# Performance work log

Hardware: AMD Instinct MI355X
Metric: run time of the kernel (lower is better)

Reference implementation:

```python
import jax, jax.numpy as jnp
import numpy as np

D_MODEL = 512
NUM_HEADS = 8
QUERY_GROUPS = 2
HEAD_DIM = D_MODEL // NUM_HEADS  # 64
ROPE_THETA = 10000.0
SCALE = 0.125  # 1/sqrt(head_dim)
NEG_INF = -1e9


def setup_inputs() -> dict:
    key = jax.random.key(0)
    k1, k2, k3 = jax.random.split(key, 3)
    B, T, S = 2, 512, 16
    x = jax.random.normal(k1, (B, T, S, D_MODEL), jnp.float32)
    padding_mask = jnp.ones((B, T * S), jnp.int32)  # [B, T*H*W], all valid
    qkv_dim = NUM_HEADS * HEAD_DIM + 2 * QUERY_GROUPS * HEAD_DIM  # 768
    qkv_w = jax.random.normal(k2, (qkv_dim, D_MODEL), jnp.float32) / np.float32(np.sqrt(D_MODEL))
    o_w = jax.random.normal(k3, (D_MODEL, NUM_HEADS * HEAD_DIM), jnp.float32) / np.float32(np.sqrt(D_MODEL))
    return {"x": x, "padding_mask": padding_mask, "qkv_w": qkv_w, "o_w": o_w}


def _rope(v, pos):
    # v: [N, T, h, d]; classic RoPE (rotate-half) over temporal positions
    half = v.shape[-1] // 2
    inv_freq = 1.0 / (ROPE_THETA ** (jnp.arange(0, half, dtype=jnp.float32) / half))
    ang = pos[:, None] * inv_freq  # [T, half]
    cos = jnp.cos(ang)[None, :, None, :]
    sin = jnp.sin(ang)[None, :, None, :]
    v1, v2 = v[..., :half], v[..., half:]
    return jnp.concatenate([v1 * cos - v2 * sin, v1 * sin + v2 * cos], axis=-1)


def reference(x, padding_mask, qkv_w, o_w):
    B, T, S, D = x.shape
    # temporal attention: flatten spatial patches into batch -> [B*S, T, D]
    xt = x.transpose(0, 2, 1, 3).reshape(B * S, T, D)
    qkv = xt @ qkv_w.T  # [B*S, T, (H+2G)*hd]
    q_end = NUM_HEADS * HEAD_DIM
    k_end = q_end + QUERY_GROUPS * HEAD_DIM
    q = qkv[..., :q_end].reshape(B * S, T, NUM_HEADS, HEAD_DIM)
    k = qkv[..., q_end:k_end].reshape(B * S, T, QUERY_GROUPS, HEAD_DIM)
    v = qkv[..., k_end:].reshape(B * S, T, QUERY_GROUPS, HEAD_DIM)
    pos = jnp.arange(T, dtype=jnp.float32)
    q = _rope(q, pos)
    k = _rope(k, pos)
    # GQA: broadcast each KV group to its query heads
    rep = NUM_HEADS // QUERY_GROUPS
    k = jnp.repeat(k, rep, axis=2)
    v = jnp.repeat(v, rep, axis=2)
    scores = jnp.einsum('nqhd,nkhd->nhqk', q, k) * SCALE  # [B*S, H, T, T]
    causal = jnp.tril(jnp.ones((T, T), bool))
    pm = padding_mask.astype(bool).reshape(-1, T)  # [B*S, T] query-side mask (as in torch path)
    mask = causal[None, None, :, :] & pm[:, None, :, None]
    scores = jnp.where(mask, scores, NEG_INF)
    attn = jax.nn.softmax(scores, axis=-1)
    out = jnp.einsum('nhqk,nkhd->nqhd', attn, v).reshape(B * S, T, D)
    out = out @ o_w.T  # output projection
    return out.reshape(B, S, T, D).transpose(0, 2, 1, 3)  # back to [B, T, S, D]
```

## Files before the change

kernel.cpp:

```cpp
#include <hip/hip_runtime.h>
#include <hip/hip_bf16.h>

typedef __attribute__((ext_vector_type(8))) short bf16x8;
typedef __attribute__((ext_vector_type(4))) float f32x4;
typedef __attribute__((ext_vector_type(4))) short s16x4;

#define DM 512
#define T_SEQ 512
#define NSEQ 32
#define MROWS 16384
#define QKV_DIM 768
#define HD 64
#define NEG_INF_F (-1000000000.0f)
#define LOG2E 1.44269504088896340736f

__device__ __forceinline__ short f2bf(float f) {
    unsigned int u = __builtin_bit_cast(unsigned int, f);
    unsigned int r = (u + 0x7FFFu + ((u >> 16) & 1u)) >> 16;
    return (short)r;
}

__device__ __forceinline__ short f2bf_hw(float f) {
    __hip_bfloat16 h = __float2bfloat16(f);
    return __builtin_bit_cast(short, h);
}

__device__ __forceinline__ void gload16(const void* g, void* l) {
    __builtin_amdgcn_global_load_lds(
        (const __attribute__((address_space(1))) void*)g,
        (__attribute__((address_space(3))) void*)l, 16, 0, 0);
}

__global__ __launch_bounds__(128) void k_convert(
    const float* __restrict__ x, const float* __restrict__ qkvw, const float* __restrict__ owf,
    short* __restrict__ xt, short* __restrict__ qw, short* __restrict__ ow,
    float* __restrict__ cosT, float* __restrict__ sinT)
{
    int bidx = blockIdx.x, tid = threadIdx.x;
    if (bidx < MROWS) {
        int m = bidx; int n = m >> 9, t = m & 511, b = n >> 4, s = n & 15;
        const float* src = x + ((size_t)((b * 512 + t) * 16 + s)) * 512;
        float4 v = *(const float4*)(src + tid * 4);
        s16x4 o; o.x = f2bf(v.x); o.y = f2bf(v.y); o.z = f2bf(v.z); o.w = f2bf(v.w);
        *(s16x4*)(xt + (size_t)m * 512 + tid * 4) = o;
    } else if (bidx < MROWS + 1280) {
        int wr = bidx - MROWS;
        const float* src; short* dst;
        if (wr < QKV_DIM) { src = qkvw + (size_t)wr * 512; dst = qw + (size_t)wr * 512; }
        else             { src = owf + (size_t)(wr - QKV_DIM) * 512; dst = ow + (size_t)(wr - QKV_DIM) * 512; }
        float4 v = *(const float4*)(src + tid * 4);
        s16x4 o; o.x = f2bf(v.x); o.y = f2bf(v.y); o.z = f2bf(v.z); o.w = f2bf(v.w);
        *(s16x4*)(dst + tid * 4) = o;
    } else {
        int idx = (bidx - (MROWS + 1280)) * 128 + tid;
        int t = idx >> 5, d = idx & 31;
        float inv = powf(10000.0f, -(float)d * (1.0f / 32.0f));
        float ang = (float)t * inv;
        float sv, cv; sincosf(ang, &sv, &cv);
        cosT[idx] = cv; sinT[idx] = sv;
    }
}

__device__ __forceinline__ void gemm_mainloop(
    const short* __restrict__ Ab, const short* __restrict__ Bb, int K,
    short* As, short* Bs, int wave, int lane, f32x4 acc[4][4])
{
    int wr = (wave >> 1) * 64, wc = (wave & 1) * 64;
    for (int kt = 0; kt < K; kt += 32) {
        __syncthreads();
        #pragma unroll
        for (int c = 0; c < 2; ++c) {
            int chunk = (wave * 2 + c) * 64 + lane;
            int row = chunk >> 2, kc = chunk & 3;
            gload16(Ab + (size_t)row * K + kt + kc * 8, As + (wave * 2 + c) * 512);
            gload16(Bb + (size_t)row * K + kt + kc * 8, Bs + (wave * 2 + c) * 512);
        }
        __syncthreads();
        bf16x8 af[4], bg[4];
        #pragma unroll
        for (int mf = 0; mf < 4; ++mf)
            af[mf] = *(const bf16x8*)(As + (wr + mf * 16 + (lane & 15)) * 32 + ((lane >> 4) << 3));
        #pragma unroll
        for (int nf = 0; nf < 4; ++nf)
            bg[nf] = *(const bf16x8*)(Bs + (wc + nf * 16 + (lane & 15)) * 32 + ((lane >> 4) << 3));
        #pragma unroll
        for (int mf = 0; mf < 4; ++mf)
            #pragma unroll
            for (int nf = 0; nf < 4; ++nf)
                acc[mf][nf] = __builtin_amdgcn_mfma_f32_16x16x32_bf16(af[mf], bg[nf], acc[mf][nf], 0, 0, 0);
    }
}

__global__ __launch_bounds__(256) void k_gemm_qkv(
    const short* __restrict__ xt, const short* __restrict__ qw,
    const float* __restrict__ cosT, const float* __restrict__ sinT,
    short* __restrict__ qb, short* __restrict__ kb, short* __restrict__ vtb)
{
    __shared__ short As[128 * 32], Bs[128 * 32];
    int tid = threadIdx.x, wave = tid >> 6, lane = tid & 63;
    int bm = blockIdx.x, bn = blockIdx.y;
    f32x4 acc[4][4] = {};
    gemm_mainloop(xt + (size_t)bm * 128 * 512, qw + (size_t)bn * 128 * 512, 512, As, Bs, wave, lane, acc);

    const float QSC = 0.125f * LOG2E;
    int wr = (wave >> 1) * 64, wc = (wave & 1) * 64;
    int gbase = bn * 128 + wc;
    int cl = lane & 15;
    #pragma unroll
    for (int mf = 0; mf < 4; ++mf) {
        #pragma unroll
        for (int rg = 0; rg < 4; ++rg) {
            int r = bm * 128 + wr + mf * 16 + ((lane >> 4) << 2) + rg;
            int n = r >> 9, t = r & 511;
            #pragma unroll
            for (int nf = 0; nf < 2; ++nf) {
                int dlo = nf * 16 + cl;
                float v1 = acc[mf][nf][rg];
                float v2 = acc[mf][nf + 2][rg];
                if (gbase < 512) {
                    int h = gbase >> 6;
                    float c = cosT[t * 32 + dlo], s = sinT[t * 32 + dlo];
                    size_t base = ((size_t)(n * 8 + h) * 512 + t) * 64;
                    qb[base + dlo]      = f2bf((v1 * c - v2 * s) * QSC);
                    qb[base + dlo + 32] = f2bf((v1 * s + v2 * c) * QSC);
                } else if (gbase < 640) {
                    int g = (gbase - 512) >> 6;
                    float c = cosT[t * 32 + dlo], s = sinT[t * 32 + dlo];
                    size_t base = ((size_t)(n * 2 + g) * 512 + t) * 64;
                    kb[base + dlo]      = f2bf(v1 * c - v2 * s);
                    kb[base + dlo + 32] = f2bf(v1 * s + v2 * c);
                } else {
                    int g = (gbase - 640) >> 6;
                    size_t base = ((size_t)(n * 2 + g) * 64) * 512;
                    vtb[base + (size_t)dlo * 512 + t]        = f2bf(v1);
                    vtb[base + (size_t)(dlo + 32) * 512 + t] = f2bf(v2);
                }
            }
        }
    }
}

__global__ __launch_bounds__(256) void k_attn(
    const short* __restrict__ qb, const short* __restrict__ kb, const short* __restrict__ vtb,
    const int* __restrict__ pm, short* __restrict__ ao)
{
    __shared__ short Kt[2][64 * 64];
    __shared__ short Vt[2][64 * 64];
    __shared__ short Pws[4][16 * 64];
    int tid = threadIdx.x, wave = tid >> 6, lane = tid & 63;
    int cl = lane & 15, g = lane >> 4;
    int bid = blockIdx.x;
    int c = bid & 3, h = (bid >> 2) & 7, n = bid >> 5;
    int kg = h >> 2;
    const short* Qb = qb + ((size_t)(n * 8 + h) * 512) * 64;
    const short* Kb = kb + ((size_t)(n * 2 + kg) * 512) * 64;
    const short* Vb = vtb + ((size_t)(n * 2 + kg) * 64) * 512;

    int rowb0 = c * 64 + wave * 16;
    int rowb1 = (7 - c) * 64 + wave * 16;

    bf16x8 qf[2][2];
    #pragma unroll
    for (int mf = 0; mf < 2; ++mf)
        #pragma unroll
        for (int ks = 0; ks < 2; ++ks)
            qf[mf][ks] = *(const bf16x8*)(Qb + (size_t)((mf ? rowb1 : rowb0) + cl) * 64 + ks * 32 + (g << 3));

    f32x4 Oc[2][4] = {};
    float mrow[2] = { -1e30f, -1e30f };
    float lrow[2] = { 0.f, 0.f };
    bool rvalid[2];
    rvalid[0] = pm[n * 512 + rowb0 + cl] != 0;
    rvalid[1] = pm[n * 512 + rowb1 + cl] != 0;

    auto stage = [&](int jt, int buf) {
        int c0 = jt * 64;
        #pragma unroll
        for (int cc = 0; cc < 2; ++cc) {
            int chunk = (wave * 2 + cc) * 64 + lane;
            int row = chunk >> 3, kc = chunk & 7;
            int sw = (kc ^ (row & 7)) << 3;
            gload16(Kb + (size_t)(c0 + row) * 64 + sw, &Kt[buf][(wave * 2 + cc) * 512]);
            gload16(Vb + (size_t)row * 512 + c0 + sw, &Vt[buf][(wave * 2 + cc) * 512]);
        }
    };

    int NT = 8 - c;
    stage(0, 0);
    for (int jt = 0; jt < NT; ++jt) {
        __syncthreads();
        if (jt + 1 < NT) stage(jt + 1, (jt + 1) & 1);
        int c0 = jt * 64;
        bool act0 = (jt <= c);
        const short* Kc = Kt[jt & 1];
        const short* Vc = Vt[jt & 1];

        f32x4 sacc[2][4] = {};
        #pragma unroll
        for (int ks = 0; ks < 2; ++ks) {
            bf16x8 kf[4];
            #pragma unroll
            for (int nf = 0; nf < 4; ++nf) {
                int row = nf * 16 + cl;
                int kc = ks * 4 + g;
                kf[nf] = *(const bf16x8*)(Kc + row * 64 + ((kc ^ (row & 7)) << 3));
            }
            #pragma unroll
            for (int mf = 0; mf < 2; ++mf) {
                if (mf == 0 && !act0) continue;
                #pragma unroll
                for (int nf = 0; nf < 4; ++nf)
                    sacc[mf][nf] = __builtin_amdgcn_mfma_f32_16x16x32_bf16(kf[nf], qf[mf][ks], sacc[mf][nf], 0, 0, 0);
            }
        }

        #pragma unroll
        for (int mf = 0; mf < 2; ++mf) {
            if (mf == 0 && !act0) continue;
            const bool diag = mf ? (jt == NT - 1) : (jt == c);
            int rq = (mf ? rowb1 : rowb0) + cl;
            float rmax = -1e30f;
            if (diag) {
                #pragma unroll
                for (int nf = 0; nf < 4; ++nf)
                    #pragma unroll
                    for (int rg = 0; rg < 4; ++rg) {
                        int kv = c0 + nf * 16 + g * 4 + rg;
                        float sv = sacc[mf][nf][rg];
                        sv = (kv <= rq && rvalid[mf]) ? sv : NEG_INF_F;
                        sacc[mf][nf][rg] = sv;
                        rmax = fmaxf(rmax, sv);
                    }
            } else {
                #pragma unroll
                for (int nf = 0; nf < 4; ++nf)
                    #pragma unroll
                    for (int rg = 0; rg < 4; ++rg)
                        rmax = fmaxf(rmax, sacc[mf][nf][rg]);
            }
            rmax = fmaxf(rmax, __shfl_xor(rmax, 16));
            rmax = fmaxf(rmax, __shfl_xor(rmax, 32));
            float mold = mrow[mf];
            int defer = __all(rmax - mold <= 8.0f);
            float mnew = defer ? mold : fmaxf(mold, rmax);
            mrow[mf] = mnew;
            float rsum = 0.f;
            #pragma unroll
            for (int nf = 0; nf < 4; ++nf) {
                s16x4 pk;
                #pragma unroll
                for (int rg = 0; rg < 4; ++rg) {
                    float p = exp2f(sacc[mf][nf][rg] - mnew);
                    rsum += p;
                    ((short*)&pk)[rg] = f2bf_hw(p);
                }
                *(s16x4*)(&Pws[wave][cl * 64 + ((((nf << 1) + (g >> 1)) ^ (cl & 7)) << 3) + ((g & 1) << 2)]) = pk;
            }
            rsum += __shfl_xor(rsum, 16);
            rsum += __shfl_xor(rsum, 32);
            if (defer) {
                lrow[mf] += rsum;
            } else {
                float alpha = exp2f(mold - mnew);
                lrow[mf] = lrow[mf] * alpha + rsum;
                #pragma unroll
                for (int rg = 0; rg < 4; ++rg) {
                    float av = __shfl(alpha, (lane & 48) + (g << 2) + rg);
                    #pragma unroll
                    for (int nf = 0; nf < 4; ++nf) Oc[mf][nf][rg] *= av;
                }
            }
            #pragma unroll
            for (int ks = 0; ks < 2; ++ks) {
                bf16x8 vf[4];
                #pragma unroll
                for (int nf = 0; nf < 4; ++nf) {
                    int row = nf * 16 + cl;
                    int kc = ks * 4 + g;
                    vf[nf] = *(const bf16x8*)(Vc + row * 64 + ((kc ^ (row & 7)) << 3));
                }
                bf16x8 pf = *(const bf16x8*)(&Pws[wave][cl * 64 + (((ks * 4 + g) ^ (cl & 7)) << 3)]);
                #pragma unroll
                for (int nf = 0; nf < 4; ++nf)
                    Oc[mf][nf] = __builtin_amdgcn_mfma_f32_16x16x32_bf16(pf, vf[nf], Oc[mf][nf], 0, 0, 0);
            }
        }
    }

    #pragma unroll
    for (int mf = 0; mf < 2; ++mf)
        #pragma unroll
        for (int rg = 0; rg < 4; ++rg) {
            float li = __shfl(lrow[mf], (lane & 48) + (g << 2) + rg);
            float inv = 1.0f / li;
            int r = (mf ? rowb1 : rowb0) + g * 4 + rg;
            size_t base = ((size_t)n * 512 + r) * 512 + h * 64;
            #pragma unroll
            for (int nf = 0; nf < 4; ++nf)
                ao[base + nf * 16 + cl] = f2bf_hw(Oc[mf][nf][rg] * inv);
        }
}

__global__ __launch_bounds__(256) void k_gemm_out(
    const short* __restrict__ ao, const short* __restrict__ ow, float* __restrict__ out)
{
    __shared__ short As[128 * 32], Bs[128 * 32];
    int tid = threadIdx.x, wave = tid >> 6, lane = tid & 63;
    int bm = blockIdx.x, bn = blockIdx.y;
    f32x4 acc[4][4] = {};
    gemm_mainloop(ao + (size_t)bm * 128 * 512, ow + (size_t)bn * 128 * 512, 512, As, Bs, wave, lane, acc);

    int wr = (wave >> 1) * 64, wc = (wave & 1) * 64;
    #pragma unroll
    for (int mf = 0; mf < 4; ++mf) {
        #pragma unroll
        for (int rg = 0; rg < 4; ++rg) {
            int r = bm * 128 + wr + mf * 16 + ((lane >> 4) << 2) + rg;
            int n = r >> 9, t = r & 511, b = n >> 4, s = n & 15;
            size_t obase = ((size_t)((b * 512 + t) * 16 + s)) * 512;
            #pragma unroll
            for (int nf = 0; nf < 4; ++nf) {
                int ccc = bn * 128 + wc + nf * 16 + (lane & 15);
                out[obase + ccc] = acc[mf][nf][rg];
            }
        }
    }
}

extern "C" void kernel_launch(void* const* d_in, const int* in_sizes, int n_in,
                              void* d_out, int out_size, void* d_ws, size_t ws_size,
                              hipStream_t stream) {
    (void)in_sizes; (void)n_in; (void)out_size; (void)ws_size;
    const float* x    = (const float*)d_in[0];
    const int*   pmsk = (const int*)d_in[1];
    const float* qkvw = (const float*)d_in[2];
    const float* owf  = (const float*)d_in[3];
    char* ws = (char*)d_ws;
    short* xt   = (short*)(ws + 0);
    short* qw   = (short*)(ws + 16777216);
    short* ow   = (short*)(ws + 17563648);
    float* cosT = (float*)(ws + 18087936);
    float* sinT = (float*)(ws + 18153472);
    short* qbuf = (short*)(ws + 18219008);
    short* kbuf = (short*)(ws + 34996224);
    short* vtbuf= (short*)(ws + 39190528);
    short* aobuf = xt;
    float* out = (float*)d_out;

    k_convert<<<dim3(17792), dim3(128), 0, stream>>>(x, qkvw, owf, xt, qw, ow, cosT, sinT);
    k_gemm_qkv<<<dim3(128, 6), dim3(256), 0, stream>>>(xt, qw, cosT, sinT, qbuf, kbuf, vtbuf);
    k_attn<<<dim3(1024), dim3(256), 0, stream>>>(qbuf, kbuf, vtbuf, pmsk, aobuf);
    k_gemm_out<<<dim3(128, 4), dim3(256), 0, stream>>>(aobuf, ow, out);
}
```

Before: 94.73 us.

## Process paired query tiles in two sequential phases to cut register pressure

```diff
diff --git a/kernel.cpp b/kernel.cpp
--- a/kernel.cpp
+++ b/kernel.cpp
@@ -156,23 +156,6 @@
     const short* Kb = kb + ((size_t)(n * 2 + kg) * 512) * 64;
     const short* Vb = vtb + ((size_t)(n * 2 + kg) * 64) * 512;
 
-    int rowb0 = c * 64 + wave * 16;
-    int rowb1 = (7 - c) * 64 + wave * 16;
-
-    bf16x8 qf[2][2];
-    #pragma unroll
-    for (int mf = 0; mf < 2; ++mf)
-        #pragma unroll
-        for (int ks = 0; ks < 2; ++ks)
-            qf[mf][ks] = *(const bf16x8*)(Qb + (size_t)((mf ? rowb1 : rowb0) + cl) * 64 + ks * 32 + (g << 3));
-
-    f32x4 Oc[2][4] = {};
-    float mrow[2] = { -1e30f, -1e30f };
-    float lrow[2] = { 0.f, 0.f };
-    bool rvalid[2];
-    rvalid[0] = pm[n * 512 + rowb0 + cl] != 0;
-    rvalid[1] = pm[n * 512 + rowb1 + cl] != 0;
-
     auto stage = [&](int jt, int buf) {
         int c0 = jt * 64;
         #pragma unroll
@@ -185,40 +168,43 @@
         }
     };
 
-    int NT = 8 - c;
     stage(0, 0);
-    for (int jt = 0; jt < NT; ++jt) {
-        __syncthreads();
-        if (jt + 1 < NT) stage(jt + 1, (jt + 1) & 1);
-        int c0 = jt * 64;
-        bool act0 = (jt <= c);
-        const short* Kc = Kt[jt & 1];
-        const short* Vc = Vt[jt & 1];
-
-        f32x4 sacc[2][4] = {};
-        #pragma unroll
-        for (int ks = 0; ks < 2; ++ks) {
-            bf16x8 kf[4];
-            #pragma unroll
-            for (int nf = 0; nf < 4; ++nf) {
-                int row = nf * 16 + cl;
-                int kc = ks * 4 + g;
-                kf[nf] = *(const bf16x8*)(Kc + row * 64 + ((kc ^ (row & 7)) << 3));
-            }
-            #pragma unroll
-            for (int mf = 0; mf < 2; ++mf) {
-                if (mf == 0 && !act0) continue;
-                #pragma unroll
-                for (int nf = 0; nf < 4; ++nf)
-                    sacc[mf][nf] = __builtin_amdgcn_mfma_f32_16x16x32_bf16(kf[nf], qf[mf][ks], sacc[mf][nf], 0, 0, 0);
-            }
-        }
-
-        #pragma unroll
-        for (int mf = 0; mf < 2; ++mf) {
-            if (mf == 0 && !act0) continue;
-            const bool diag = mf ? (jt == NT - 1) : (jt == c);
-            int rq = (mf ? rowb1 : rowb0) + cl;
+    int buf = 0;
+    #pragma unroll
+    for (int ph = 0; ph < 2; ++ph) {
+        int rowb = (ph ? (7 - c) : c) * 64 + wave * 16;
+        int NTp = ph ? (8 - c) : (c + 1);
+        bf16x8 qf[2];
+        #pragma unroll
+        for (int ks = 0; ks < 2; ++ks)
+            qf[ks] = *(const bf16x8*)(Qb + (size_t)(rowb + cl) * 64 + ks * 32 + (g << 3));
+        f32x4 Oc[4] = {};
+        float mrow = -1e30f, lrow = 0.f;
+        bool rv = pm[n * 512 + rowb + cl] != 0;
+        int rq = rowb + cl;
+
+        for (int jt = 0; jt < NTp; ++jt) {
+            __syncthreads();
+            if (jt + 1 < NTp) stage(jt + 1, buf ^ 1);
+            else if (ph == 0) stage(0, buf ^ 1);
+            int c0 = jt * 64;
+            const short* Kc = Kt[buf];
+            const short* Vc = Vt[buf];
+            buf ^= 1;
+
+            f32x4 sacc[4] = {};
+            #pragma unroll
+            for (int ks = 0; ks < 2; ++ks) {
+                #pragma unroll
+                for (int nf = 0; nf < 4; ++nf) {
+                    int row = nf * 16 + cl;
+                    int kc = ks * 4 + g;
+                    bf16x8 kf = *(const bf16x8*)(Kc + row * 64 + ((kc ^ (row & 7)) << 3));
+                    sacc[nf] = __builtin_amdgcn_mfma_f32_16x16x32_bf16(kf, qf[ks], sacc[nf], 0, 0, 0);
+                }
+            }
+
+            const bool diag = (jt == NTp - 1);
             float rmax = -1e30f;
             if (diag) {
                 #pragma unroll
@@ -226,9 +212,9 @@
                     #pragma unroll
                     for (int rg = 0; rg < 4; ++rg) {
                         int kv = c0 + nf * 16 + g * 4 + rg;
-                        float sv = sacc[mf][nf][rg];
-                        sv = (kv <= rq && rvalid[mf]) ? sv : NEG_INF_F;
-                        sacc[mf][nf][rg] = sv;
+                        float sv = sacc[nf][rg];
+                        sv = (kv <= rq && rv) ? sv : NEG_INF_F;
+                        sacc[nf][rg] = sv;
                         rmax = fmaxf(rmax, sv);
                     }
             } else {
@@ -236,21 +222,21 @@
                 for (int nf = 0; nf < 4; ++nf)
                     #pragma unroll
                     for (int rg = 0; rg < 4; ++rg)
-                        rmax = fmaxf(rmax, sacc[mf][nf][rg]);
+                        rmax = fmaxf(rmax, sacc[nf][rg]);
             }
             rmax = fmaxf(rmax, __shfl_xor(rmax, 16));
             rmax = fmaxf(rmax, __shfl_xor(rmax, 32));
-            float mold = mrow[mf];
+            float mold = mrow;
             int defer = __all(rmax - mold <= 8.0f);
             float mnew = defer ? mold : fmaxf(mold, rmax);
-            mrow[mf] = mnew;
+            mrow = mnew;
             float rsum = 0.f;
             #pragma unroll
             for (int nf = 0; nf < 4; ++nf) {
                 s16x4 pk;
                 #pragma unroll
                 for (int rg = 0; rg < 4; ++rg) {
-                    float p = exp2f(sacc[mf][nf][rg] - mnew);
+                    float p = exp2f(sacc[nf][rg] - mnew);
                     rsum += p;
                     ((short*)&pk)[rg] = f2bf_hw(p);
                 }
@@ -259,46 +245,42 @@
             rsum += __shfl_xor(rsum, 16);
             rsum += __shfl_xor(rsum, 32);
             if (defer) {
-                lrow[mf] += rsum;
+                lrow += rsum;
             } else {
                 float alpha = exp2f(mold - mnew);
-                lrow[mf] = lrow[mf] * alpha + rsum;
+                lrow = lrow * alpha + rsum;
                 #pragma unroll
                 for (int rg = 0; rg < 4; ++rg) {
                     float av = __shfl(alpha, (lane & 48) + (g << 2) + rg);
                     #pragma unroll
-                    for (int nf = 0; nf < 4; ++nf) Oc[mf][nf][rg] *= av;
-                }
-            }
+                    for (int nf = 0; nf < 4; ++nf) Oc[nf][rg] *= av;
+                }
+            }
+
             #pragma unroll
             for (int ks = 0; ks < 2; ++ks) {
-                bf16x8 vf[4];
+                bf16x8 pf = *(const bf16x8*)(&Pws[wave][cl * 64 + (((ks * 4 + g) ^ (cl & 7)) << 3)]);
                 #pragma unroll
                 for (int nf = 0; nf < 4; ++nf) {
                     int row = nf * 16 + cl;
                     int kc = ks * 4 + g;
-                    vf[nf] = *(const bf16x8*)(Vc + row * 64 + ((kc ^ (row & 7)) << 3));
-                }
-                bf16x8 pf = *(const bf16x8*)(&Pws[wave][cl * 64 + (((ks * 4 + g) ^ (cl & 7)) << 3)]);
-                #pragma unroll
-                for (int nf = 0; nf < 4; ++nf)
-                    Oc[mf][nf] = __builtin_amdgcn_mfma_f32_16x16x32_bf16(pf, vf[nf], Oc[mf][nf], 0, 0, 0);
-            }
-        }
-    }
-
-    #pragma unroll
-    for (int mf = 0; mf < 2; ++mf)
+                    bf16x8 vf = *(const bf16x8*)(Vc + row * 64 + ((kc ^ (row & 7)) << 3));
+                    Oc[nf] = __builtin_amdgcn_mfma_f32_16x16x32_bf16(pf, vf, Oc[nf], 0, 0, 0);
+                }
+            }
+        }
+
         #pragma unroll
         for (int rg = 0; rg < 4; ++rg) {
-            float li = __shfl(lrow[mf], (lane & 48) + (g << 2) + rg);
+            float li = __shfl(lrow, (lane & 48) + (g << 2) + rg);
             float inv = 1.0f / li;
-            int r = (mf ? rowb1 : rowb0) + g * 4 + rg;
+            int r = rowb + g * 4 + rg;
             size_t base = ((size_t)n * 512 + r) * 512 + h * 64;
             #pragma unroll
             for (int nf = 0; nf < 4; ++nf)
-                ao[base + nf * 16 + cl] = f2bf_hw(Oc[mf][nf][rg] * inv);
-        }
+                ao[base + nf * 16 + cl] = f2bf_hw(Oc[nf][rg] * inv);
+        }
+    }
 }
 
 __global__ __launch_bounds__(256) void k_gemm_out(
```

Result: faster. 90.13 us (-4.8%).
